# Optimization experiments

Hardware: AMD Instinct MI355X
Metric: run time of the kernel (lower is better)

The kernel has to match this reference:

```python
import jax, jax.numpy as jnp
import numpy as np

N_NODES = 100000
N_EDGES = 1600000
D_IN = 64
D_OUT = 64


def setup_inputs() -> dict:
    key = jax.random.key(0)
    k1, k2, k3, k4 = jax.random.split(key, 4)
    feat = jax.random.normal(k1, (N_NODES, D_IN), dtype=jnp.float32)
    edge_src = jax.random.randint(k2, (N_EDGES,), 0, N_NODES, dtype=jnp.int64)
    edge_dst = jax.random.randint(k3, (N_EDGES,), 0, N_NODES, dtype=jnp.int64)
    # xavier_uniform with gain for relu (sqrt(2)) on [out, in] Linear weight
    gain = float(np.sqrt(2.0))
    limit = gain * float(np.sqrt(6.0 / (D_IN + D_OUT)))
    fc_weight = jax.random.uniform(k4, (D_OUT, D_IN), dtype=jnp.float32,
                                   minval=-limit, maxval=limit)
    return {"feat": feat, "edge_src": edge_src, "edge_dst": edge_dst,
            "fc_weight": fc_weight}


def reference(feat, edge_src, edge_dst, fc_weight):
    # SDDMM: edge score a_e = <h_src, h_dst>  (fn.u_dot_v)
    h_src = feat[edge_src]                      # [E, d]
    h_dst = feat[edge_dst]                      # [E, d]
    a = jnp.sum(h_src * h_dst, axis=-1, keepdims=True)  # [E, 1]
    # SpMM: neigh[v] = sum_{(u->v)} h_u * a_e  (u_mul_e + sum)
    m = h_src * a                               # [E, d]
    neigh = jax.ops.segment_sum(m, edge_dst, num_segments=feat.shape[0])  # [N, d]
    # Linear without bias: y = neigh @ W.T
    return neigh @ fc_weight.T
```

## Files before the change

### kernel.cpp

```cpp
#include <hip/hip_runtime.h>

#define N_NODES 100000
#define N_EDGES 1600000
#define D 64
#define NB 782
#define CAP 3072
#define EPB 8192
#define NPART ((N_EDGES + EPB - 1) / EPB)
#define RSH 14

typedef unsigned short ushort_t;
typedef unsigned int uint_t;

__device__ __forceinline__ ushort_t f2bf(float f) {
    uint_t u = __float_as_uint(f);
    u += 0x7FFF + ((u >> 16) & 1);
    return (ushort_t)(u >> 16);
}

__global__ __launch_bounds__(256) void repack_init(const float* __restrict__ feat,
                                                   ushort_t* __restrict__ featb,
                                                   int* __restrict__ gcur) {
    const int tid = blockIdx.x * 256 + threadIdx.x;
    if (tid < NB) gcur[tid] = tid * CAP;
    const int base = tid * 16;
    if (base >= N_NODES * D) return;
    const float4* f4 = (const float4*)(feat + base);
    ushort4* o4 = (ushort4*)(featb + base);
#pragma unroll
    for (int j = 0; j < 4; ++j) {
        const float4 v = f4[j];
        o4[j] = make_ushort4(f2bf(v.x), f2bf(v.y), f2bf(v.z), f2bf(v.w));
    }
}

__global__ __launch_bounds__(1024) void partition(const int* __restrict__ esrc,
                                                  const int* __restrict__ edst,
                                                  int* __restrict__ gcur,
                                                  int* __restrict__ slab) {
    __shared__ int stage[EPB];
    __shared__ ushort_t bkt16[EPB];
    __shared__ int cnt[NB];
    __shared__ int cur[NB];
    __shared__ int gb[NB];
    __shared__ int s[1024];
    const int t = threadIdx.x;
    const int base = blockIdx.x * EPB;
    const int n = min(EPB, N_EDGES - base);

    if (t < NB) cnt[t] = 0;
    __syncthreads();
    for (int i = t; i < n; i += 1024)
        atomicAdd(&cnt[edst[base + i] >> 7], 1);
    __syncthreads();
    const int v = (t < NB) ? cnt[t] : 0;
    s[t] = v;
    __syncthreads();
    for (int off = 1; off < 1024; off <<= 1) {
        const int x = (t >= off) ? s[t - off] : 0;
        __syncthreads();
        s[t] += x;
        __syncthreads();
    }
    if (t < NB) {
        const int excl = s[t] - v;
        cur[t] = excl;
        gb[t] = (v ? atomicAdd(&gcur[t], v) : 0) - excl;
    }
    __syncthreads();
    for (int i = t; i < n; i += 1024) {
        const int d = edst[base + i];
        const int bkt = d >> 7;
        const int pos = atomicAdd(&cur[bkt], 1);
        stage[pos] = ((d & 127) << 17) | esrc[base + i];
        bkt16[pos] = (ushort_t)bkt;
    }
    __syncthreads();
    for (int i = t; i < n; i += 1024) {
        const int bkt = bkt16[i];
        const int gp = gb[bkt] + i;
        if (gp < (bkt + 1) * CAP)
            slab[gp] = stage[i];
    }
}

template<int CTRL>
__device__ __forceinline__ float fadd_dpp(float x) {
    const int r = __builtin_amdgcn_update_dpp(0, __float_as_int(x), CTRL, 0xF, 0xF, true);
    return x + __int_as_float(r);
}
__device__ __forceinline__ float red8(float p) {
    p = fadd_dpp<0xB1>(p);
    p = fadd_dpp<0x4E>(p);
    p = fadd_dpp<0x141>(p);
    return p;
}

__device__ __forceinline__ void cvt8(const uint4 u, float* __restrict__ g) {
    g[0] = __uint_as_float(u.x << 16); g[1] = __uint_as_float(u.x & 0xFFFF0000u);
    g[2] = __uint_as_float(u.y << 16); g[3] = __uint_as_float(u.y & 0xFFFF0000u);
    g[4] = __uint_as_float(u.z << 16); g[5] = __uint_as_float(u.z & 0xFFFF0000u);
    g[6] = __uint_as_float(u.w << 16); g[7] = __uint_as_float(u.w & 0xFFFF0000u);
}
__device__ __forceinline__ float cvt_dot(const uint4 u, const float* __restrict__ h,
                                         float* __restrict__ g) {
    cvt8(u, g);
    float p = 0.f;
#pragma unroll
    for (int k = 0; k < 8; ++k) p += g[k] * h[k];
    return p;
}

__global__ __launch_bounds__(512) void fused_spmm_gemm(
    const uint4* __restrict__ featb4,
    const int* __restrict__ slab,
    const int* __restrict__ gcur,
    const float* __restrict__ W,
    float* __restrict__ out)
{
    __shared__ __align__(16) char ovl[32768];
    __shared__ int seB[CAP];
    __shared__ int rowoff[129];
    int* seA     = (int*)ovl;
    int* kcnt    = (int*)(ovl + 12288);
    int* kcur    = (int*)(ovl + 16384);
    int* s       = (int*)(ovl + 20480);
    float* accs  = (float*)ovl;
    float4* accs4 = (float4*)ovl;

    const int t = threadIdx.x;
    const int b = blockIdx.x;
    const int nbase = b << 7;
    const int nb_nodes = min(128, N_NODES - nbase);
    const int sbase = b * CAP;
    const int ne = min(gcur[b] - sbase, CAP);

    for (int i = t; i < ne; i += 512) seA[i] = slab[sbase + i];
    kcnt[t] = 0; kcnt[t + 512] = 0;
    __syncthreads();
    for (int i = t; i < ne; i += 512) {
        const int pk = seA[i];
        atomicAdd(&kcnt[((pk >> 17) << 3) | ((pk & 0x1FFFF) >> RSH)], 1);
    }
    __syncthreads();
    const int v0 = kcnt[2 * t], v1 = kcnt[2 * t + 1];
    const int sum = v0 + v1;
    s[t] = sum;
    __syncthreads();
    for (int off = 1; off < 512; off <<= 1) {
        const int x = (t >= off) ? s[t - off] : 0;
        __syncthreads();
        s[t] += x;
        __syncthreads();
    }
    const int excl = s[t] - sum;
    kcur[2 * t] = excl;
    kcur[2 * t + 1] = excl + v0;
    __syncthreads();
    if (t < 128) rowoff[t] = kcur[t << 3];
    if (t == 0) rowoff[128] = ne;
    __syncthreads();
    for (int i = t; i < ne; i += 512) {
        const int pk = seA[i];
        const int key = ((pk >> 17) << 3) | ((pk & 0x1FFFF) >> RSH);
        const int pos = atomicAdd(&kcur[key], 1);
        seB[pos] = pk & 0x1FFFF;
    }
    __syncthreads();

    const int slot = t >> 3;
    const int l = t & 7;
#pragma unroll
    for (int ln0 = 0; ln0 < 128; ln0 += 64) {
        const int ln = ln0 + slot;
        if (ln >= nb_nodes) continue;
        const int nidx = nbase + ln;
        float h[8];
        cvt8(featb4[nidx * 8 + l], h);
        float acc[8];
#pragma unroll
        for (int k = 0; k < 8; ++k) acc[k] = 0.f;

        int e = rowoff[ln];
        const int e1 = rowoff[ln + 1];
        for (; e + 3 < e1; e += 4) {
            const int s0 = seB[e], s1 = seB[e + 1], s2 = seB[e + 2], s3 = seB[e + 3];
            const uint4 u0 = featb4[s0 * 8 + l];
            const uint4 u1 = featb4[s1 * 8 + l];
            const uint4 u2 = featb4[s2 * 8 + l];
            const uint4 u3 = featb4[s3 * 8 + l];
            float g0[8], g1[8], g2[8], g3[8];
            float p0 = cvt_dot(u0, h, g0);
            float p1 = cvt_dot(u1, h, g1);
            float p2 = cvt_dot(u2, h, g2);
            float p3 = cvt_dot(u3, h, g3);
            p0 = red8(p0); p1 = red8(p1); p2 = red8(p2); p3 = red8(p3);
#pragma unroll
            for (int k = 0; k < 8; ++k)
                acc[k] += g0[k] * p0 + g1[k] * p1 + g2[k] * p2 + g3[k] * p3;
        }
        for (; e < e1; ++e) {
            const uint4 u0 = featb4[seB[e] * 8 + l];
            float g0[8];
            float p0 = red8(cvt_dot(u0, h, g0));
#pragma unroll
            for (int k = 0; k < 8; ++k) acc[k] += g0[k] * p0;
        }
        accs4[ln * 16 + 2 * l]     = make_float4(acc[0], acc[1], acc[2], acc[3]);
        accs4[ln * 16 + 2 * l + 1] = make_float4(acc[4], acc[5], acc[6], acc[7]);
    }
    __syncthreads();

    const int o = t & 63;
    const int rg = t >> 6;
    float wcol[D];
    {
        const float4* W4 = (const float4*)(W + o * D);
#pragma unroll
        for (int i4 = 0; i4 < 16; ++i4) {
            const float4 w = W4[i4];
            wcol[4 * i4 + 0] = w.x; wcol[4 * i4 + 1] = w.y;
            wcol[4 * i4 + 2] = w.z; wcol[4 * i4 + 3] = w.w;
        }
    }
    for (int r = rg; r < nb_nodes; r += 8) {
        const float4* arow = (const float4*)&accs[r * D];
        float sumv = 0.f;
#pragma unroll
        for (int i4 = 0; i4 < 16; ++i4) {
            const float4 a4 = arow[i4];
            sumv += a4.x * wcol[4 * i4 + 0];
            sumv += a4.y * wcol[4 * i4 + 1];
            sumv += a4.z * wcol[4 * i4 + 2];
            sumv += a4.w * wcol[4 * i4 + 3];
        }
        out[(nbase + r) * D + o] = sumv;
    }
}

extern "C" void kernel_launch(void* const* d_in, const int* in_sizes, int n_in,
                              void* d_out, int out_size, void* d_ws, size_t ws_size,
                              hipStream_t stream) {
    const float* feat = (const float*)d_in[0];
    const int*   esrc = (const int*)d_in[1];
    const int*   edst = (const int*)d_in[2];
    const float* W    = (const float*)d_in[3];
    float* out = (float*)d_out;

    char* ws = (char*)d_ws;
    ushort_t* featb = (ushort_t*)(ws);
    int* slab = (int*)(ws + 12800000);
    int* gcur = (int*)(ws + 12800000 + (size_t)NB * CAP * 4);

    repack_init<<<(N_NODES * D / 16 + 255) / 256, 256, 0, stream>>>(feat, featb, gcur);
    partition<<<NPART, 1024, 0, stream>>>(esrc, edst, gcur, slab);
    fused_spmm_gemm<<<NB, 512, 0, stream>>>((const uint4*)featb, slab, gcur, W, out);
}
```

Before: 203.0 us.

## Shrink node buckets to 64, merge repack into partition, split GEMM into own kernel

Destination buckets shrink from 128 to 64 nodes, so the SpMM grid runs more, smaller blocks (256 threads) with less shared memory each. The per-row sub-sort by source range is dropped. The bf16 repack is merged into the partition launch as extra blocks, and a memset replaces the counter init. The fused GEMM is split out: SpMM writes neighbour sums to the output buffer in global memory, and a separate kernel reads them back and applies W in place. This adds a full round trip of the node-feature matrix through global memory and loses source-locality ordering within rows.

```diff
diff --git a/kernel.cpp b/kernel.cpp
--- a/kernel.cpp
+++ b/kernel.cpp
@@ -3,11 +3,12 @@
 #define N_NODES 100000
 #define N_EDGES 1600000
 #define D 64
-#define NB 782
-#define CAP 3072
-#define EPB 8192
-#define NPART ((N_EDGES + EPB - 1) / EPB)
-#define RSH 14
+#define BK 64
+#define NB2 1563
+#define CAP2 1280
+#define EPB 4096
+#define NPART 391
+#define NREPACK 782
 
 typedef unsigned short ushort_t;
 typedef unsigned int uint_t;
@@ -18,68 +19,81 @@
     return (ushort_t)(u >> 16);
 }
 
-__global__ __launch_bounds__(256) void repack_init(const float* __restrict__ feat,
+__global__ __launch_bounds__(512) void part_repack(const float* __restrict__ feat,
                                                    ushort_t* __restrict__ featb,
-                                                   int* __restrict__ gcur) {
-    const int tid = blockIdx.x * 256 + threadIdx.x;
-    if (tid < NB) gcur[tid] = tid * CAP;
-    const int base = tid * 16;
-    if (base >= N_NODES * D) return;
-    const float4* f4 = (const float4*)(feat + base);
-    ushort4* o4 = (ushort4*)(featb + base);
-#pragma unroll
-    for (int j = 0; j < 4; ++j) {
-        const float4 v = f4[j];
-        o4[j] = make_ushort4(f2bf(v.x), f2bf(v.y), f2bf(v.z), f2bf(v.w));
-    }
-}
-
-__global__ __launch_bounds__(1024) void partition(const int* __restrict__ esrc,
-                                                  const int* __restrict__ edst,
-                                                  int* __restrict__ gcur,
-                                                  int* __restrict__ slab) {
+                                                   const int* __restrict__ esrc,
+                                                   const int* __restrict__ edst,
+                                                   int* __restrict__ gcur,
+                                                   int* __restrict__ slab) {
     __shared__ int stage[EPB];
     __shared__ ushort_t bkt16[EPB];
-    __shared__ int cnt[NB];
-    __shared__ int cur[NB];
-    __shared__ int gb[NB];
-    __shared__ int s[1024];
+    __shared__ int cnt[NB2];
+    __shared__ int cur[NB2];
+    __shared__ int gb[NB2];
+    __shared__ int s[512];
     const int t = threadIdx.x;
+
+    if (blockIdx.x >= NPART) {
+        const int idx = (blockIdx.x - NPART) * 512 + t;
+        const int base = idx * 16;
+        if (base < N_NODES * D) {
+            const float4* f4 = (const float4*)(feat + base);
+            ushort4* o4 = (ushort4*)(featb + base);
+#pragma unroll
+            for (int j = 0; j < 4; ++j) {
+                const float4 v = f4[j];
+                o4[j] = make_ushort4(f2bf(v.x), f2bf(v.y), f2bf(v.z), f2bf(v.w));
+            }
+        }
+        return;
+    }
+
     const int base = blockIdx.x * EPB;
     const int n = min(EPB, N_EDGES - base);
 
-    if (t < NB) cnt[t] = 0;
-    __syncthreads();
-    for (int i = t; i < n; i += 1024)
-        atomicAdd(&cnt[edst[base + i] >> 7], 1);
-    __syncthreads();
-    const int v = (t < NB) ? cnt[t] : 0;
-    s[t] = v;
-    __syncthreads();
-    for (int off = 1; off < 1024; off <<= 1) {
+    for (int i = t; i < NB2; i += 512) cnt[i] = 0;
+    __syncthreads();
+    for (int i = t; i < n; i += 512)
+        atomicAdd(&cnt[edst[base + i] >> 6], 1);
+    __syncthreads();
+    int c0 = 0, c1 = 0, c2 = 0, c3 = 0;
+    {
+        const int k = 4 * t;
+        if (k + 0 < NB2) c0 = cnt[k + 0];
+        if (k + 1 < NB2) c1 = cnt[k + 1];
+        if (k + 2 < NB2) c2 = cnt[k + 2];
+        if (k + 3 < NB2) c3 = cnt[k + 3];
+    }
+    const int sum = c0 + c1 + c2 + c3;
+    s[t] = sum;
+    __syncthreads();
+    for (int off = 1; off < 512; off <<= 1) {
         const int x = (t >= off) ? s[t - off] : 0;
         __syncthreads();
         s[t] += x;
         __syncthreads();
     }
-    if (t < NB) {
-        const int excl = s[t] - v;
-        cur[t] = excl;
-        gb[t] = (v ? atomicAdd(&gcur[t], v) : 0) - excl;
-    }
-    __syncthreads();
-    for (int i = t; i < n; i += 1024) {
+    int run = s[t] - sum;
+    {
+        const int k = 4 * t;
+        if (k + 0 < NB2) { cur[k+0] = run; gb[k+0] = (c0 ? atomicAdd(&gcur[k+0], c0) : 0) + (k+0)*CAP2 - run; run += c0; }
+        if (k + 1 < NB2) { cur[k+1] = run; gb[k+1] = (c1 ? atomicAdd(&gcur[k+1], c1) : 0) + (k+1)*CAP2 - run; run += c1; }
+        if (k + 2 < NB2) { cur[k+2] = run; gb[k+2] = (c2 ? atomicAdd(&gcur[k+2], c2) : 0) + (k+2)*CAP2 - run; run += c2; }
+        if (k + 3 < NB2) { cur[k+3] = run; gb[k+3] = (c3 ? atomicAdd(&gcur[k+3], c3) : 0) + (k+3)*CAP2 - run; run += c3; }
+    }
+    __syncthreads();
+    for (int i = t; i < n; i += 512) {
         const int d = edst[base + i];
-        const int bkt = d >> 7;
+        const int bkt = d >> 6;
         const int pos = atomicAdd(&cur[bkt], 1);
-        stage[pos] = ((d & 127) << 17) | esrc[base + i];
+        stage[pos] = ((d & 63) << 17) | esrc[base + i];
         bkt16[pos] = (ushort_t)bkt;
     }
     __syncthreads();
-    for (int i = t; i < n; i += 1024) {
+    for (int i = t; i < n; i += 512) {
         const int bkt = bkt16[i];
         const int gp = gb[bkt] + i;
-        if (gp < (bkt + 1) * CAP)
+        if (gp < (bkt + 1) * CAP2)
             slab[gp] = stage[i];
     }
 }
@@ -111,59 +125,45 @@
     return p;
 }
 
-__global__ __launch_bounds__(512) void fused_spmm_gemm(
-    const uint4* __restrict__ featb4,
-    const int* __restrict__ slab,
-    const int* __restrict__ gcur,
-    const float* __restrict__ W,
-    float* __restrict__ out)
-{
-    __shared__ __align__(16) char ovl[32768];
-    __shared__ int seB[CAP];
-    __shared__ int rowoff[129];
-    int* seA     = (int*)ovl;
-    int* kcnt    = (int*)(ovl + 12288);
-    int* kcur    = (int*)(ovl + 16384);
-    int* s       = (int*)(ovl + 20480);
-    float* accs  = (float*)ovl;
-    float4* accs4 = (float4*)ovl;
-
+__global__ __launch_bounds__(256) void fused_spmm(const uint4* __restrict__ featb4,
+                                                  const int* __restrict__ slab,
+                                                  const int* __restrict__ gcur,
+                                                  float4* __restrict__ neigh4) {
+    __shared__ int seA[CAP2];
+    __shared__ int seB[CAP2];
+    __shared__ int kcnt[64];
+    __shared__ int kcur[64];
+    __shared__ int rowoff[65];
     const int t = threadIdx.x;
     const int b = blockIdx.x;
-    const int nbase = b << 7;
-    const int nb_nodes = min(128, N_NODES - nbase);
-    const int sbase = b * CAP;
-    const int ne = min(gcur[b] - sbase, CAP);
-
-    for (int i = t; i < ne; i += 512) seA[i] = slab[sbase + i];
-    kcnt[t] = 0; kcnt[t + 512] = 0;
-    __syncthreads();
-    for (int i = t; i < ne; i += 512) {
+    const int nbase = b * BK;
+    const int nb_nodes = min(BK, N_NODES - nbase);
+    const int sbase = b * CAP2;
+    const int ne = min(gcur[b], CAP2);
+
+    for (int i = t; i < ne; i += 256) seA[i] = slab[sbase + i];
+    if (t < 64) kcnt[t] = 0;
+    __syncthreads();
+    for (int i = t; i < ne; i += 256)
+        atomicAdd(&kcnt[seA[i] >> 17], 1);
+    __syncthreads();
+    const int v = (t < 64) ? kcnt[t] : 0;
+    if (t < 64) kcur[t] = v;
+    __syncthreads();
+    for (int off = 1; off < 64; off <<= 1) {
+        const int x = (t >= off && t < 64) ? kcur[t - off] : 0;
+        __syncthreads();
+        if (t < 64) kcur[t] += x;
+        __syncthreads();
+    }
+    if (t < 64) rowoff[t] = kcur[t] - v;
+    if (t == 0) rowoff[64] = ne;
+    __syncthreads();
+    if (t < 64) kcur[t] = rowoff[t];
+    __syncthreads();
+    for (int i = t; i < ne; i += 256) {
         const int pk = seA[i];
-        atomicAdd(&kcnt[((pk >> 17) << 3) | ((pk & 0x1FFFF) >> RSH)], 1);
-    }
-    __syncthreads();
-    const int v0 = kcnt[2 * t], v1 = kcnt[2 * t + 1];
-    const int sum = v0 + v1;
-    s[t] = sum;
-    __syncthreads();
-    for (int off = 1; off < 512; off <<= 1) {
-        const int x = (t >= off) ? s[t - off] : 0;
-        __syncthreads();
-        s[t] += x;
-        __syncthreads();
-    }
-    const int excl = s[t] - sum;
-    kcur[2 * t] = excl;
-    kcur[2 * t + 1] = excl + v0;
-    __syncthreads();
-    if (t < 128) rowoff[t] = kcur[t << 3];
-    if (t == 0) rowoff[128] = ne;
-    __syncthreads();
-    for (int i = t; i < ne; i += 512) {
-        const int pk = seA[i];
-        const int key = ((pk >> 17) << 3) | ((pk & 0x1FFFF) >> RSH);
-        const int pos = atomicAdd(&kcur[key], 1);
+        const int pos = atomicAdd(&kcur[pk >> 17], 1);
         seB[pos] = pk & 0x1FFFF;
     }
     __syncthreads();
@@ -171,7 +171,7 @@
     const int slot = t >> 3;
     const int l = t & 7;
 #pragma unroll
-    for (int ln0 = 0; ln0 < 128; ln0 += 64) {
+    for (int ln0 = 0; ln0 < BK; ln0 += 32) {
         const int ln = ln0 + slot;
         if (ln >= nb_nodes) continue;
         const int nidx = nbase + ln;
@@ -206,35 +206,41 @@
 #pragma unroll
             for (int k = 0; k < 8; ++k) acc[k] += g0[k] * p0;
         }
-        accs4[ln * 16 + 2 * l]     = make_float4(acc[0], acc[1], acc[2], acc[3]);
-        accs4[ln * 16 + 2 * l + 1] = make_float4(acc[4], acc[5], acc[6], acc[7]);
-    }
-    __syncthreads();
-
+        neigh4[nidx * 16 + 2 * l]     = make_float4(acc[0], acc[1], acc[2], acc[3]);
+        neigh4[nidx * 16 + 2 * l + 1] = make_float4(acc[4], acc[5], acc[6], acc[7]);
+    }
+}
+
+__global__ __launch_bounds__(256) void gemm_bcast(float* __restrict__ out,
+                                                  const float* __restrict__ W) {
+    const int t = threadIdx.x;
     const int o = t & 63;
     const int rg = t >> 6;
+    const int base = blockIdx.x * BK;
+    const int rows = min(BK, N_NODES - base);
+
     float wcol[D];
     {
         const float4* W4 = (const float4*)(W + o * D);
 #pragma unroll
         for (int i4 = 0; i4 < 16; ++i4) {
             const float4 w = W4[i4];
-            wcol[4 * i4 + 0] = w.x; wcol[4 * i4 + 1] = w.y;
-            wcol[4 * i4 + 2] = w.z; wcol[4 * i4 + 3] = w.w;
-        }
-    }
-    for (int r = rg; r < nb_nodes; r += 8) {
-        const float4* arow = (const float4*)&accs[r * D];
+            wcol[4*i4+0] = w.x; wcol[4*i4+1] = w.y;
+            wcol[4*i4+2] = w.z; wcol[4*i4+3] = w.w;
+        }
+    }
+    for (int r = rg; r < rows; r += 4) {
+        const float4* arow = (const float4*)(out + (long)(base + r) * D);
         float sumv = 0.f;
 #pragma unroll
         for (int i4 = 0; i4 < 16; ++i4) {
             const float4 a4 = arow[i4];
-            sumv += a4.x * wcol[4 * i4 + 0];
-            sumv += a4.y * wcol[4 * i4 + 1];
-            sumv += a4.z * wcol[4 * i4 + 2];
-            sumv += a4.w * wcol[4 * i4 + 3];
-        }
-        out[(nbase + r) * D + o] = sumv;
+            sumv += a4.x * wcol[4*i4+0];
+            sumv += a4.y * wcol[4*i4+1];
+            sumv += a4.z * wcol[4*i4+2];
+            sumv += a4.w * wcol[4*i4+3];
+        }
+        out[(long)(base + r) * D + o] = sumv;
     }
 }
 
@@ -250,9 +256,10 @@
     char* ws = (char*)d_ws;
     ushort_t* featb = (ushort_t*)(ws);
     int* slab = (int*)(ws + 12800000);
-    int* gcur = (int*)(ws + 12800000 + (size_t)NB * CAP * 4);
-
-    repack_init<<<(N_NODES * D / 16 + 255) / 256, 256, 0, stream>>>(feat, featb, gcur);
-    partition<<<NPART, 1024, 0, stream>>>(esrc, edst, gcur, slab);
-    fused_spmm_gemm<<<NB, 512, 0, stream>>>((const uint4*)featb, slab, gcur, W, out);
-}
+    int* gcur = (int*)(ws + 12800000 + (size_t)NB2 * CAP2 * 4);
+
+    hipMemsetAsync(gcur, 0, NB2 * sizeof(int), stream);
+    part_repack<<<NPART + NREPACK, 512, 0, stream>>>(feat, featb, esrc, edst, gcur, slab);
+    fused_spmm<<<NB2, 256, 0, stream>>>((const uint4*)featb, slab, gcur, (float4*)out);
+    gemm_bcast<<<NB2, 256, 0, stream>>>(out, W);
+}
```

Result: slower. 233.3 us (+14.9%).
